# Kernel optimization log

Measured on AMD Instinct MI355X. Metric: run time of the kernel, lower is better.

## Reference

```python
import jax, jax.numpy as jnp
import numpy as np

NUM_HEADS = 16

def setup_inputs() -> dict:
    key = jax.random.key(0)
    k1, k2, k3 = jax.random.split(key, 3)
    B, N, C = 2, 2048, 1024
    x = jax.random.normal(k1, (B, N, C), dtype=jnp.float32)
    w_qkv = jax.random.normal(k2, (C, 3 * C), dtype=jnp.float32) * (C ** -0.5)
    w_proj = jax.random.normal(k3, (C, C), dtype=jnp.float32) * (C ** -0.5)
    b_proj = jnp.zeros((C,), dtype=jnp.float32)
    return {"x": x, "w_qkv": w_qkv, "w_proj": w_proj, "b_proj": b_proj}

def reference(x, w_qkv, w_proj, b_proj):
    B, N, C = x.shape
    H = NUM_HEADS
    D = C // H
    scale = D ** -0.5
    qkv = (x @ w_qkv).reshape(B, N, 3, H, D).transpose(2, 0, 3, 1, 4)  # [3,B,H,N,D]
    q, k, v = qkv[0], qkv[1], qkv[2]
    attn = jnp.einsum("bhnd,bhmd->bhnm", q, k) * scale  # [B,H,N,N]
    attn = jax.nn.softmax(attn, axis=-1)
    out = jnp.einsum("bhnm,bhmd->bhnd", attn, v)  # [B,H,N,D]
    out = out.transpose(0, 2, 1, 3).reshape(B, N, C)
    return out @ w_proj + b_proj
```

## Files before the change

### kernel.cpp

```cpp
#include <hip/hip_runtime.h>
#include <hip/hip_bf16.h>
#include <math.h>

#define B_SZ   2
#define N_SEQ  2048
#define C_DIM  1024
#define H_NUM  16
#define D_HEAD 64
#define M_ROWS (B_SZ * N_SEQ)
#define QKV_N  (3 * C_DIM)

typedef __attribute__((ext_vector_type(8))) short  bf16x8;
typedef __attribute__((ext_vector_type(4))) float  floatx4;

static __device__ __forceinline__ unsigned short f2bf(float x) {
    unsigned int u = __float_as_uint(x);
    u = (u + 0x7FFFu + ((u >> 16) & 1u)) >> 16;
    return (unsigned short)u;
}
static __device__ __forceinline__ unsigned int f2bf_hi(float x) {
    unsigned int u = __float_as_uint(x);
    return u + 0x7FFFu + ((u >> 16) & 1u);
}

#if __has_builtin(__builtin_amdgcn_exp2f)
#define EXP2F(x) __builtin_amdgcn_exp2f(x)
#else
#define EXP2F(x) exp2f(x)
#endif

#define GLP(p) ((const __attribute__((address_space(1))) void*)(p))
#define LDP(p) ((__attribute__((address_space(3))) void*)(p))

#define CEXP 0.18033688011112042f

__global__ __launch_bounds__(256)
void prep_fused(const float* __restrict__ x,      unsigned short* __restrict__ xb,
                const float* __restrict__ w_qkv,  unsigned short* __restrict__ wqkvT,
                const float* __restrict__ w_proj, unsigned short* __restrict__ wprojT)
{
    __shared__ unsigned short t[64][72];
    const int bid = blockIdx.x;
    const int tid = threadIdx.x;

    if (bid < 4096) {
        const int i = bid * 256 + tid;
        float4 v = ((const float4*)x)[i];
        ushort4 p;
        p.x = f2bf(v.x); p.y = f2bf(v.y); p.z = f2bf(v.z); p.w = f2bf(v.w);
        ((ushort4*)xb)[i] = p;
        return;
    }

    const float* W;
    unsigned short* WT;
    int N, tt;
    if (bid < 4096 + 768) { W = w_qkv;  WT = wqkvT;  N = QKV_N; tt = bid - 4096; }
    else                  { W = w_proj; WT = wprojT; N = C_DIM; tt = bid - 4864; }
    const int ntiles = N / 64;
    const int n0 = (tt % ntiles) * 64;
    const int k0 = (tt / ntiles) * 64;
    const int K  = C_DIM;

    const int tc = tid & 15;
    const int tr = tid >> 4;
    #pragma unroll
    for (int p = 0; p < 4; ++p) {
        const int r = tr + p * 16;
        float4 v = *(const float4*)&W[(size_t)(k0 + r) * N + n0 + tc * 4];
        ushort4 pk;
        pk.x = f2bf(v.x); pk.y = f2bf(v.y); pk.z = f2bf(v.z); pk.w = f2bf(v.w);
        *(ushort4*)&t[r][tc * 4] = pk;
    }
    __syncthreads();

    const int n  = tid >> 2;
    const int c0 = (tid & 3) * 16;
    unsigned short tmp[16];
    #pragma unroll
    for (int i = 0; i < 16; ++i) tmp[i] = t[c0 + i][n];
    *(uint4*)&WT[(size_t)(n0 + n) * K + k0 + c0]     = *(uint4*)&tmp[0];
    *(uint4*)&WT[(size_t)(n0 + n) * K + k0 + c0 + 8] = *(uint4*)&tmp[8];
}

__global__ __launch_bounds__(256)
void gemm_qkv(const unsigned short* __restrict__ A,
              const unsigned short* __restrict__ BT,
              unsigned short* __restrict__ qbuf,
              unsigned short* __restrict__ kbuf,
              unsigned short* __restrict__ vbuf)
{
    const int K = C_DIM;
    __shared__ unsigned short As[128 * 32];
    __shared__ unsigned short Bs[128 * 32];

    const int tid  = threadIdx.x;
    const int lane = tid & 63;
    const int wave = tid >> 6;
    const int l15  = lane & 15;
    const int lq   = lane >> 4;
    const int wm   = (wave & 1) * 64;
    const int wn   = (wave >> 1) * 64;

    const int bm = blockIdx.y * 128;
    const int bn = blockIdx.x * 128;
    const bool isv = (bn >= 2 * C_DIM);

    const int sr = tid >> 2;
    const int sc = (tid & 3) * 8;

    const unsigned short* ga0 = A  + (size_t)(bm + sr) * K + sc;
    const unsigned short* ga1 = A  + (size_t)(bm + 64 + sr) * K + sc;
    const unsigned short* gb0 = BT + (size_t)(bn + sr) * K + sc;
    const unsigned short* gb1 = BT + (size_t)(bn + 64 + sr) * K + sc;

    unsigned short* la0 = &As[sr * 32 + sc];
    unsigned short* la1 = &As[(64 + sr) * 32 + sc];
    unsigned short* lb0 = &Bs[sr * 32 + sc];
    unsigned short* lb1 = &Bs[(64 + sr) * 32 + sc];

    floatx4 acc[4][4];
    #pragma unroll
    for (int i = 0; i < 4; ++i)
        #pragma unroll
        for (int j = 0; j < 4; ++j) acc[i][j] = (floatx4){0.f, 0.f, 0.f, 0.f};

    for (int kt = 0; kt < K; kt += 32) {
        __builtin_amdgcn_global_load_lds(GLP(ga0), LDP(la0), 16, 0, 0);
        __builtin_amdgcn_global_load_lds(GLP(ga1), LDP(la1), 16, 0, 0);
        __builtin_amdgcn_global_load_lds(GLP(gb0), LDP(lb0), 16, 0, 0);
        __builtin_amdgcn_global_load_lds(GLP(gb1), LDP(lb1), 16, 0, 0);
        ga0 += 32; ga1 += 32; gb0 += 32; gb1 += 32;
        __syncthreads();

        bf16x8 af[4], bfr[4];
        #pragma unroll
        for (int t = 0; t < 4; ++t) {
            af[t]  = *(const bf16x8*)&As[(wm + t * 16 + l15) * 32 + lq * 8];
            bfr[t] = *(const bf16x8*)&Bs[(wn + t * 16 + l15) * 32 + lq * 8];
        }
        if (isv) {
            #pragma unroll
            for (int mt = 0; mt < 4; ++mt)
                #pragma unroll
                for (int nt = 0; nt < 4; ++nt)
                    acc[mt][nt] = __builtin_amdgcn_mfma_f32_16x16x32_bf16(
                        af[mt], bfr[nt], acc[mt][nt], 0, 0, 0);
        } else {
            #pragma unroll
            for (int mt = 0; mt < 4; ++mt)
                #pragma unroll
                for (int nt = 0; nt < 4; ++nt)
                    acc[mt][nt] = __builtin_amdgcn_mfma_f32_16x16x32_bf16(
                        bfr[nt], af[mt], acc[mt][nt], 0, 0, 0);
        }
        __syncthreads();
    }

    if (!isv) {
        const bool isq = (bn < C_DIM);
        const float scq = isq ? CEXP : 1.0f;
        unsigned short* dbuf = isq ? qbuf : kbuf;
        #pragma unroll
        for (int nt = 0; nt < 4; ++nt) {
            const int colb = bn + wn + nt * 16 + lq * 4;
            const int h    = (colb >> 6) & 15;
            const int d    = colb & 63;
            #pragma unroll
            for (int mt = 0; mt < 4; ++mt) {
                const int row = bm + wm + mt * 16 + l15;
                const int b   = row >> 11;
                const int n   = row & 2047;
                ushort4 pk;
                pk.x = f2bf(acc[mt][nt][0] * scq);
                pk.y = f2bf(acc[mt][nt][1] * scq);
                pk.z = f2bf(acc[mt][nt][2] * scq);
                pk.w = f2bf(acc[mt][nt][3] * scq);
                *(ushort4*)&dbuf[((size_t)(b * H_NUM + h) * N_SEQ + n) * D_HEAD + d] = pk;
            }
        }
    } else {
        #pragma unroll
        for (int nt = 0; nt < 4; ++nt) {
            const int col = bn + wn + nt * 16 + l15;
            const int h   = (col >> 6) & 15;
            const int d   = col & 63;
            #pragma unroll
            for (int mt = 0; mt < 4; ++mt) {
                const int row = bm + wm + mt * 16 + lq * 4;
                const int b   = row >> 11;
                const int n   = row & 2047;
                const int a   = n & 63;
                const int fk  = (a & 0x20) | ((a & 0x0C) << 1) | ((a & 0x10) >> 2);
                ushort4 pk;
                pk.x = f2bf(acc[mt][nt][0]); pk.y = f2bf(acc[mt][nt][1]);
                pk.z = f2bf(acc[mt][nt][2]); pk.w = f2bf(acc[mt][nt][3]);
                *(ushort4*)&vbuf[((size_t)(b * H_NUM + h) * D_HEAD + d) * N_SEQ
                                 + (n & ~63) + fk] = pk;
            }
        }
    }
}

__global__ __launch_bounds__(256)
void attn_mfma(const unsigned short* __restrict__ qbuf,
               const unsigned short* __restrict__ kbuf,
               const unsigned short* __restrict__ vbuf,
               unsigned short* __restrict__ attnb)
{
    __shared__ unsigned short KsS[2][64 * 64];
    __shared__ unsigned short VtS[2][64 * 64];

    const int tid  = threadIdx.x;
    const int lane = tid & 63;
    const int wave = tid >> 6;
    const int l15  = lane & 15;
    const int lq   = lane >> 4;
    const int e    = l15 & 7;

    const int bid  = blockIdx.x;
    const int bh   = (bid & 7) * 4 + (bid >> 8);
    const int qblk = (bid >> 3) & 31;
    const int b    = bh >> 4;
    const int h    = bh & 15;
    const int q0   = qblk * 64 + wave * 16;

    const unsigned short* khead = kbuf + (size_t)bh * N_SEQ * D_HEAD;
    const unsigned short* vhead = vbuf + (size_t)bh * D_HEAD * N_SEQ;

    bf16x8 qf[2];
    {
        const unsigned short* qrow = qbuf
            + ((size_t)bh * N_SEQ + q0 + l15) * D_HEAD + lq * 8;
        qf[0] = *(const bf16x8*)qrow;
        qf[1] = *(const bf16x8*)(qrow + 32);
    }

    floatx4 acc[4];
    #pragma unroll
    for (int dc = 0; dc < 4; ++dc) acc[dc] = (floatx4){0.f, 0.f, 0.f, 0.f};
    float lsum = 0.f;

    const int srow = tid >> 3;
    const int gso  = ((tid & 7) ^ (srow & 7)) * 8;

    __builtin_amdgcn_global_load_lds(GLP(khead + (size_t)srow * 64 + gso),
                                     LDP(&KsS[0][tid * 8]), 16, 0, 0);
    __builtin_amdgcn_global_load_lds(GLP(khead + (size_t)(srow + 32) * 64 + gso),
                                     LDP(&KsS[0][2048 + tid * 8]), 16, 0, 0);
    __builtin_amdgcn_global_load_lds(GLP(vhead + (size_t)srow * N_SEQ + gso),
                                     LDP(&VtS[0][tid * 8]), 16, 0, 0);
    __builtin_amdgcn_global_load_lds(GLP(vhead + (size_t)(srow + 32) * N_SEQ + gso),
                                     LDP(&VtS[0][2048 + tid * 8]), 16, 0, 0);

    for (int tile = 0; tile < N_SEQ / 64; ++tile) {
        const int cur = tile & 1;
        __syncthreads();

        if (tile + 1 < N_SEQ / 64) {
            const int m1 = (tile + 1) * 64;
            const int nx = cur ^ 1;
            __builtin_amdgcn_global_load_lds(GLP(khead + (size_t)(m1 + srow) * 64 + gso),
                                             LDP(&KsS[nx][tid * 8]), 16, 0, 0);
            __builtin_amdgcn_global_load_lds(GLP(khead + (size_t)(m1 + srow + 32) * 64 + gso),
                                             LDP(&KsS[nx][2048 + tid * 8]), 16, 0, 0);
            __builtin_amdgcn_global_load_lds(GLP(vhead + (size_t)srow * N_SEQ + m1 + gso),
                                             LDP(&VtS[nx][tid * 8]), 16, 0, 0);
            __builtin_amdgcn_global_load_lds(GLP(vhead + (size_t)(srow + 32) * N_SEQ + m1 + gso),
                                             LDP(&VtS[nx][2048 + tid * 8]), 16, 0, 0);
        }

        const unsigned short* Ksc = &KsS[cur][0];
        const unsigned short* Vtc = &VtS[cur][0];

        floatx4 st[4];
        #pragma unroll
        for (int t = 0; t < 4; ++t) {
            bf16x8 k0 = *(const bf16x8*)&Ksc[(t * 16 + l15) * 64 + ((lq ^ e) * 8)];
            bf16x8 k1 = *(const bf16x8*)&Ksc[(t * 16 + l15) * 64 + (((4 + lq) ^ e) * 8)];
            floatx4 s = (floatx4){-8.f, -8.f, -8.f, -8.f};
            s = __builtin_amdgcn_mfma_f32_16x16x32_bf16(k0, qf[0], s, 0, 0, 0);
            s = __builtin_amdgcn_mfma_f32_16x16x32_bf16(k1, qf[1], s, 0, 0, 0);
            st[t] = s;
        }

        unsigned int pk[8];
        float la = 0.f;
        #pragma unroll
        for (int t = 0; t < 4; ++t) {
            float p0 = EXP2F(st[t][0]);
            float p1 = EXP2F(st[t][1]);
            float p2 = EXP2F(st[t][2]);
            float p3 = EXP2F(st[t][3]);
            la += (p0 + p1) + (p2 + p3);
            pk[t * 2]     = __builtin_amdgcn_perm(f2bf_hi(p1), f2bf_hi(p0), 0x07060302u);
            pk[t * 2 + 1] = __builtin_amdgcn_perm(f2bf_hi(p3), f2bf_hi(p2), 0x07060302u);
        }
        lsum += la;
        union { uint4 u; bf16x8 v; } cvt0, cvt1;
        cvt0.u = make_uint4(pk[0], pk[1], pk[2], pk[3]);
        cvt1.u = make_uint4(pk[4], pk[5], pk[6], pk[7]);

        #pragma unroll
        for (int dc = 0; dc < 4; ++dc) {
            bf16x8 v0 = *(const bf16x8*)&Vtc[(dc * 16 + l15) * 64 + ((lq ^ e) * 8)];
            bf16x8 v1 = *(const bf16x8*)&Vtc[(dc * 16 + l15) * 64 + (((4 + lq) ^ e) * 8)];
            acc[dc] = __builtin_amdgcn_mfma_f32_16x16x32_bf16(v0, cvt0.v, acc[dc], 0, 0, 0);
            acc[dc] = __builtin_amdgcn_mfma_f32_16x16x32_bf16(v1, cvt1.v, acc[dc], 0, 0, 0);
        }
    }

    float l = lsum;
    l += __shfl_xor(l, 16, 64);
    l += __shfl_xor(l, 32, 64);
    const float inv = 1.f / l;
    const int q = q0 + l15;
    unsigned short* orow = attnb + ((size_t)b * N_SEQ + q) * C_DIM + h * D_HEAD;
    #pragma unroll
    for (int dc = 0; dc < 4; ++dc) {
        ushort4 pkk;
        pkk.x = f2bf(acc[dc][0] * inv);
        pkk.y = f2bf(acc[dc][1] * inv);
        pkk.z = f2bf(acc[dc][2] * inv);
        pkk.w = f2bf(acc[dc][3] * inv);
        *(ushort4*)&orow[dc * 16 + lq * 4] = pkk;
    }
}

__global__ __launch_bounds__(256)
void gemm_bt(const unsigned short* __restrict__ A,
             const unsigned short* __restrict__ BT,
             const float* __restrict__ bias,
             float* __restrict__ Cm,
             int M, int N, int K)
{
    __shared__ unsigned short As[128 * 32];
    __shared__ unsigned short Bs[64 * 32];

    const int tid  = threadIdx.x;
    const int lane = tid & 63;
    const int wave = tid >> 6;
    const int l15  = lane & 15;
    const int lq   = lane >> 4;
    const int wm   = (wave & 1) * 64;
    const int wn   = (wave >> 1) * 32;

    const int bm = blockIdx.y * 128;
    const int bn = blockIdx.x * 64;

    const int sr = tid >> 2;
    const int sc = (tid & 3) * 8;

    const unsigned short* ga0 = A  + (size_t)(bm + sr) * K + sc;
    const unsigned short* ga1 = A  + (size_t)(bm + 64 + sr) * K + sc;
    const unsigned short* gb0 = BT + (size_t)(bn + sr) * K + sc;

    unsigned short* la0 = &As[sr * 32 + sc];
    unsigned short* la1 = &As[(64 + sr) * 32 + sc];
    unsigned short* lb0 = &Bs[sr * 32 + sc];

    floatx4 acc[4][2];
    #pragma unroll
    for (int i = 0; i < 4; ++i)
        #pragma unroll
        for (int j = 0; j < 2; ++j) acc[i][j] = (floatx4){0.f, 0.f, 0.f, 0.f};

    for (int kt = 0; kt < K; kt += 32) {
        __builtin_amdgcn_global_load_lds(GLP(ga0), LDP(la0), 16, 0, 0);
        __builtin_amdgcn_global_load_lds(GLP(ga1), LDP(la1), 16, 0, 0);
        __builtin_amdgcn_global_load_lds(GLP(gb0), LDP(lb0), 16, 0, 0);
        ga0 += 32; ga1 += 32; gb0 += 32;
        __syncthreads();

        bf16x8 af[4], bfr[2];
        #pragma unroll
        for (int t = 0; t < 4; ++t)
            af[t] = *(const bf16x8*)&As[(wm + t * 16 + l15) * 32 + lq * 8];
        #pragma unroll
        for (int t = 0; t < 2; ++t)
            bfr[t] = *(const bf16x8*)&Bs[(wn + t * 16 + l15) * 32 + lq * 8];
        #pragma unroll
        for (int mt = 0; mt < 4; ++mt)
            #pragma unroll
            for (int nt = 0; nt < 2; ++nt)
                acc[mt][nt] = __builtin_amdgcn_mfma_f32_16x16x32_bf16(
                    af[mt], bfr[nt], acc[mt][nt], 0, 0, 0);
        __syncthreads();
    }

    float bv[2];
    #pragma unroll
    for (int nt = 0; nt < 2; ++nt) bv[nt] = bias[bn + wn + nt * 16 + l15];
    #pragma unroll
    for (int mt = 0; mt < 4; ++mt) {
        const int row = bm + wm + mt * 16 + lq * 4;
        #pragma unroll
        for (int nt = 0; nt < 2; ++nt) {
            const int col = bn + wn + nt * 16 + l15;
            #pragma unroll
            for (int r = 0; r < 4; ++r)
                Cm[(size_t)(row + r) * N + col] = acc[mt][nt][r] + bv[nt];
        }
    }
}

extern "C" void kernel_launch(void* const* d_in, const int* in_sizes, int n_in,
                              void* d_out, int out_size, void* d_ws, size_t ws_size,
                              hipStream_t stream)
{
    const float* x      = (const float*)d_in[0];
    const float* w_qkv  = (const float*)d_in[1];
    const float* w_proj = (const float*)d_in[2];
    const float* b_proj = (const float*)d_in[3];
    float*       out    = (float*)d_out;

    unsigned short* xb     = (unsigned short*)d_ws;
    unsigned short* wqkvT  = xb     + (size_t)M_ROWS * C_DIM;
    unsigned short* wprojT = wqkvT  + (size_t)QKV_N * C_DIM;
    unsigned short* qbuf   = wprojT + (size_t)C_DIM * C_DIM;
    unsigned short* kbuf   = qbuf   + (size_t)M_ROWS * C_DIM;
    unsigned short* vbuf   = kbuf   + (size_t)M_ROWS * C_DIM;
    unsigned short* attnb  = vbuf   + (size_t)M_ROWS * C_DIM;

    prep_fused<<<4096 + 768 + 256, 256, 0, stream>>>(x, xb, w_qkv, wqkvT, w_proj, wprojT);

    gemm_qkv<<<dim3(QKV_N / 128, M_ROWS / 128), 256, 0, stream>>>(xb, wqkvT, qbuf, kbuf, vbuf);

    attn_mfma<<<1024, 256, 0, stream>>>(qbuf, kbuf, vbuf, attnb);

    gemm_bt<<<dim3(C_DIM / 64, M_ROWS / 128), 256, 0, stream>>>(
        attnb, wprojT, b_proj, out, M_ROWS, C_DIM, C_DIM);
}
```

Measured before the change: 208.9 us.

## Double attention query block per workgroup, unify QKV epilogue, use packed bf16 convert

The attention kernel now launches 512 blocks of 512 threads, each covering 128 query rows. Each 64-row K/V tile staged in LDS is therefore shared by twice as many waves, and each thread issues one async load per operand instead of two. The QKV GEMM drops its V-versus-QK operand-swap branch: all tiles use one MFMA ordering, and Q/K are written with scalar strided stores instead of packed 4-wide stores. Softmax probabilities are packed to bf16 with the hardware cvt_pk instruction when it is available. The trade-offs are fewer resident blocks and more scattered Q/K stores in exchange for halved K/V traffic per query row.

```diff
diff --git a/kernel.cpp b/kernel.cpp
--- a/kernel.cpp
+++ b/kernel.cpp
@@ -22,6 +22,18 @@
     unsigned int u = __float_as_uint(x);
     return u + 0x7FFFu + ((u >> 16) & 1u);
 }
+#if __has_builtin(__builtin_amdgcn_cvt_pk_bf16_f32)
+typedef __bf16 bf16_2 __attribute__((ext_vector_type(2)));
+static __device__ __forceinline__ unsigned int pkbf(float a, float b) {
+    union { bf16_2 v; unsigned int u; } c;
+    c.v = __builtin_amdgcn_cvt_pk_bf16_f32(a, b);
+    return c.u;
+}
+#else
+static __device__ __forceinline__ unsigned int pkbf(float a, float b) {
+    return __builtin_amdgcn_perm(f2bf_hi(b), f2bf_hi(a), 0x07060302u);
+}
+#endif
 
 #if __has_builtin(__builtin_amdgcn_exp2f)
 #define EXP2F(x) __builtin_amdgcn_exp2f(x)
@@ -104,7 +116,6 @@
 
     const int bm = blockIdx.y * 128;
     const int bn = blockIdx.x * 128;
-    const bool isv = (bn >= 2 * C_DIM);
 
     const int sr = tid >> 2;
     const int sc = (tid & 3) * 8;
@@ -139,70 +150,48 @@
             af[t]  = *(const bf16x8*)&As[(wm + t * 16 + l15) * 32 + lq * 8];
             bfr[t] = *(const bf16x8*)&Bs[(wn + t * 16 + l15) * 32 + lq * 8];
         }
-        if (isv) {
+        #pragma unroll
+        for (int mt = 0; mt < 4; ++mt)
             #pragma unroll
-            for (int mt = 0; mt < 4; ++mt)
+            for (int nt = 0; nt < 4; ++nt)
+                acc[mt][nt] = __builtin_amdgcn_mfma_f32_16x16x32_bf16(
+                    af[mt], bfr[nt], acc[mt][nt], 0, 0, 0);
+        __syncthreads();
+    }
+
+    #pragma unroll
+    for (int nt = 0; nt < 4; ++nt) {
+        const int col  = bn + wn + nt * 16 + l15;
+        const int reg3 = col >> 10;
+        const int h    = (col >> 6) & 15;
+        const int d    = col & 63;
+        const float sc4 = (reg3 == 0) ? CEXP : 1.0f;
+        #pragma unroll
+        for (int mt = 0; mt < 4; ++mt) {
+            const int row = bm + wm + mt * 16 + lq * 4;
+            const int b   = row >> 11;
+            const int n   = row & 2047;
+            if (reg3 < 2) {
+                unsigned short* dst = (reg3 ? kbuf : qbuf)
+                    + ((size_t)(b * H_NUM + h) * N_SEQ + n) * D_HEAD + d;
                 #pragma unroll
-                for (int nt = 0; nt < 4; ++nt)
-                    acc[mt][nt] = __builtin_amdgcn_mfma_f32_16x16x32_bf16(
-                        af[mt], bfr[nt], acc[mt][nt], 0, 0, 0);
-        } else {
-            #pragma unroll
-            for (int mt = 0; mt < 4; ++mt)
-                #pragma unroll
-                for (int nt = 0; nt < 4; ++nt)
-                    acc[mt][nt] = __builtin_amdgcn_mfma_f32_16x16x32_bf16(
-                        bfr[nt], af[mt], acc[mt][nt], 0, 0, 0);
-        }
-        __syncthreads();
-    }
-
-    if (!isv) {
-        const bool isq = (bn < C_DIM);
-        const float scq = isq ? CEXP : 1.0f;
-        unsigned short* dbuf = isq ? qbuf : kbuf;
-        #pragma unroll
-        for (int nt = 0; nt < 4; ++nt) {
-            const int colb = bn + wn + nt * 16 + lq * 4;
-            const int h    = (colb >> 6) & 15;
-            const int d    = colb & 63;
-            #pragma unroll
-            for (int mt = 0; mt < 4; ++mt) {
-                const int row = bm + wm + mt * 16 + l15;
-                const int b   = row >> 11;
-                const int n   = row & 2047;
-                ushort4 pk;
-                pk.x = f2bf(acc[mt][nt][0] * scq);
-                pk.y = f2bf(acc[mt][nt][1] * scq);
-                pk.z = f2bf(acc[mt][nt][2] * scq);
-                pk.w = f2bf(acc[mt][nt][3] * scq);
-                *(ushort4*)&dbuf[((size_t)(b * H_NUM + h) * N_SEQ + n) * D_HEAD + d] = pk;
-            }
-        }
-    } else {
-        #pragma unroll
-        for (int nt = 0; nt < 4; ++nt) {
-            const int col = bn + wn + nt * 16 + l15;
-            const int h   = (col >> 6) & 15;
-            const int d   = col & 63;
-            #pragma unroll
-            for (int mt = 0; mt < 4; ++mt) {
-                const int row = bm + wm + mt * 16 + lq * 4;
-                const int b   = row >> 11;
-                const int n   = row & 2047;
-                const int a   = n & 63;
-                const int fk  = (a & 0x20) | ((a & 0x0C) << 1) | ((a & 0x10) >> 2);
+                for (int r = 0; r < 4; ++r)
+                    dst[(size_t)r * D_HEAD] = f2bf(acc[mt][nt][r] * sc4);
+            } else {
+                const int a  = n & 63;
+                const int fk = (a & 0x20) | ((a & 0x0C) << 1) | ((a & 0x10) >> 2);
+                unsigned short* dst = vbuf
+                    + ((size_t)(b * H_NUM + h) * D_HEAD + d) * N_SEQ + (n & ~63) + fk;
                 ushort4 pk;
                 pk.x = f2bf(acc[mt][nt][0]); pk.y = f2bf(acc[mt][nt][1]);
                 pk.z = f2bf(acc[mt][nt][2]); pk.w = f2bf(acc[mt][nt][3]);
-                *(ushort4*)&vbuf[((size_t)(b * H_NUM + h) * D_HEAD + d) * N_SEQ
-                                 + (n & ~63) + fk] = pk;
+                *(ushort4*)dst = pk;
             }
         }
     }
 }
 
-__global__ __launch_bounds__(256)
+__global__ __launch_bounds__(512)
 void attn_mfma(const unsigned short* __restrict__ qbuf,
                const unsigned short* __restrict__ kbuf,
                const unsigned short* __restrict__ vbuf,
@@ -219,11 +208,11 @@
     const int e    = l15 & 7;
 
     const int bid  = blockIdx.x;
-    const int bh   = (bid & 7) * 4 + (bid >> 8);
-    const int qblk = (bid >> 3) & 31;
+    const int bh   = (bid & 7) * 4 + (bid >> 7);
+    const int qblk = (bid >> 3) & 15;
     const int b    = bh >> 4;
     const int h    = bh & 15;
-    const int q0   = qblk * 64 + wave * 16;
+    const int q0   = qblk * 128 + wave * 16;
 
     const unsigned short* khead = kbuf + (size_t)bh * N_SEQ * D_HEAD;
     const unsigned short* vhead = vbuf + (size_t)bh * D_HEAD * N_SEQ;
@@ -246,12 +235,8 @@
 
     __builtin_amdgcn_global_load_lds(GLP(khead + (size_t)srow * 64 + gso),
                                      LDP(&KsS[0][tid * 8]), 16, 0, 0);
-    __builtin_amdgcn_global_load_lds(GLP(khead + (size_t)(srow + 32) * 64 + gso),
-                                     LDP(&KsS[0][2048 + tid * 8]), 16, 0, 0);
     __builtin_amdgcn_global_load_lds(GLP(vhead + (size_t)srow * N_SEQ + gso),
                                      LDP(&VtS[0][tid * 8]), 16, 0, 0);
-    __builtin_amdgcn_global_load_lds(GLP(vhead + (size_t)(srow + 32) * N_SEQ + gso),
-                                     LDP(&VtS[0][2048 + tid * 8]), 16, 0, 0);
 
     for (int tile = 0; tile < N_SEQ / 64; ++tile) {
         const int cur = tile & 1;
@@ -262,12 +247,8 @@
             const int nx = cur ^ 1;
             __builtin_amdgcn_global_load_lds(GLP(khead + (size_t)(m1 + srow) * 64 + gso),
                                              LDP(&KsS[nx][tid * 8]), 16, 0, 0);
-            __builtin_amdgcn_global_load_lds(GLP(khead + (size_t)(m1 + srow + 32) * 64 + gso),
-                                             LDP(&KsS[nx][2048 + tid * 8]), 16, 0, 0);
             __builtin_amdgcn_global_load_lds(GLP(vhead + (size_t)srow * N_SEQ + m1 + gso),
                                              LDP(&VtS[nx][tid * 8]), 16, 0, 0);
-            __builtin_amdgcn_global_load_lds(GLP(vhead + (size_t)(srow + 32) * N_SEQ + m1 + gso),
-                                             LDP(&VtS[nx][2048 + tid * 8]), 16, 0, 0);
         }
 
         const unsigned short* Ksc = &KsS[cur][0];
@@ -293,8 +274,8 @@
             float p2 = EXP2F(st[t][2]);
             float p3 = EXP2F(st[t][3]);
             la += (p0 + p1) + (p2 + p3);
-            pk[t * 2]     = __builtin_amdgcn_perm(f2bf_hi(p1), f2bf_hi(p0), 0x07060302u);
-            pk[t * 2 + 1] = __builtin_amdgcn_perm(f2bf_hi(p3), f2bf_hi(p2), 0x07060302u);
+            pk[t * 2]     = pkbf(p0, p1);
+            pk[t * 2 + 1] = pkbf(p2, p3);
         }
         lsum += la;
         union { uint4 u; bf16x8 v; } cvt0, cvt1;
@@ -426,7 +407,7 @@
 
     gemm_qkv<<<dim3(QKV_N / 128, M_ROWS / 128), 256, 0, stream>>>(xb, wqkvT, qbuf, kbuf, vbuf);
 
-    attn_mfma<<<1024, 256, 0, stream>>>(qbuf, kbuf, vbuf, attnb);
+    attn_mfma<<<512, 512, 0, stream>>>(qbuf, kbuf, vbuf, attnb);
 
     gemm_bt<<<dim3(C_DIM / 64, M_ROWS / 128), 256, 0, stream>>>(
         attnb, wprojT, b_proj, out, M_ROWS, C_DIM, C_DIM);
```

Result: faster. 201.3 us (-3.6%).
